# Optimization experiments

Hardware: AMD Instinct MI355X
Metric: run time of the kernel (lower is better)

The kernel has to match this reference:

```python
import jax, jax.numpy as jnp
import numpy as np
from jax.ops import segment_sum

HID = 64
B = 512  # number of graphs


def gcn(x, W, b, src, dst, n):
    # PyG GCNConv: h = xW; add self-loops; symmetric norm D^-1/2 A_hat D^-1/2; + bias
    h = x @ W
    deg = 1.0 + segment_sum(jnp.ones_like(src, dtype=h.dtype), dst, num_segments=n)
    dinv = deg ** -0.5
    msg = h[src] * (dinv[src] * dinv[dst])[:, None]          # [E, out]
    out = segment_sum(msg, dst, num_segments=n) + h * (dinv * dinv)[:, None]
    return out + b


def mean_pool(x, batch, nb):
    s = segment_sum(x, batch, num_segments=nb)
    cnt = segment_sum(jnp.ones_like(batch, dtype=x.dtype), batch, num_segments=nb)
    return s / jnp.maximum(cnt, 1.0)[:, None]


def branch(x, ei, batch, params):
    (W1, b1, W2, b2, W3, b3) = params
    n = x.shape[0]
    src, dst = ei[0], ei[1]
    x = jax.nn.relu(gcn(x, W1, b1, src, dst, n))
    x = jax.nn.relu(gcn(x, W2, b2, src, dst, n))
    x = jax.nn.relu(gcn(x, W3, b3, src, dst, n))
    return mean_pool(x, batch, B)


def setup_inputs() -> dict:
    key = jax.random.key(0)
    ks = jax.random.split(key, 24)
    s = 0.05
    d = {
        'p_x': jax.random.normal(ks[0], (200000, 41), jnp.float32),
        'p_edge_index': jax.random.randint(ks[1], (2, 800000), 0, 200000, jnp.int32),
        'p_batch': jnp.sort(jax.random.randint(ks[2], (200000,), 0, B, jnp.int32)),
        'l_x': jax.random.normal(ks[3], (100000, 78), jnp.float32),
        'l_edge_index': jax.random.randint(ks[4], (2, 400000), 0, 100000, jnp.int32),
        'l_batch': jnp.sort(jax.random.randint(ks[5], (100000,), 0, B, jnp.int32)),
    }
    def lin(k, i, o):
        return jax.random.normal(k, (i, o), jnp.float32) * s
    d['p_W1'] = lin(ks[6], 41, HID);      d['p_b1'] = jnp.zeros((HID,))
    d['p_W2'] = lin(ks[7], HID, 2*HID);   d['p_b2'] = jnp.zeros((2*HID,))
    d['p_W3'] = lin(ks[8], 2*HID, 4*HID); d['p_b3'] = jnp.zeros((4*HID,))
    d['l_W1'] = lin(ks[9], 78, HID);      d['l_b1'] = jnp.zeros((HID,))
    d['l_W2'] = lin(ks[10], HID, 2*HID);  d['l_b2'] = jnp.zeros((2*HID,))
    d['l_W3'] = lin(ks[11], 2*HID, 4*HID); d['l_b3'] = jnp.zeros((4*HID,))
    d['fc1_W'] = lin(ks[12], 8*HID, 1024); d['fc1_b'] = jnp.zeros((1024,))
    d['fc2_W'] = lin(ks[13], 1024, 512);   d['fc2_b'] = jnp.zeros((512,))
    d['out_W'] = lin(ks[14], 512, 1);      d['out_b'] = jnp.zeros((1,))
    return d


def reference(p_x, p_edge_index, p_batch, l_x, l_edge_index, l_batch,
              p_W1, p_b1, p_W2, p_b2, p_W3, p_b3,
              l_W1, l_b1, l_W2, l_b2, l_W3, l_b3,
              fc1_W, fc1_b, fc2_W, fc2_b, out_W, out_b):
    p = branch(p_x, p_edge_index, p_batch, (p_W1, p_b1, p_W2, p_b2, p_W3, p_b3))
    l = branch(l_x, l_edge_index, l_batch, (l_W1, l_b1, l_W2, l_b2, l_W3, l_b3))
    x = jnp.concatenate([p, l], axis=1)                      # [B, 512]
    x = jax.nn.relu(x @ fc1_W + fc1_b)
    # dropout is identity in eval mode
    x = jax.nn.relu(x @ fc2_W + fc2_b)
    return x @ out_W + out_b                                  # [B, 1]
```

## Files before the change

### kernel.cpp

```cpp
#include <hip/hip_runtime.h>

typedef __attribute__((ext_vector_type(8))) short short8;
typedef __attribute__((ext_vector_type(16))) float f32x16;


__device__ __forceinline__ unsigned short f2bf_rne(float f) {
  unsigned u = __float_as_uint(f);
  u += 0x7fffu + ((u >> 16) & 1u);
  return (unsigned short)(u >> 16);
}
__device__ __forceinline__ float bf2f(unsigned short h) {
  return __uint_as_float(((unsigned)h) << 16);
}


static __global__ void k_fill(float* __restrict__ p, float v, int n) {
  int i = blockIdx.x * blockDim.x + threadIdx.x;
  if (i < n) p[i] = v;
}

static __global__ void k_deg(float* __restrict__ deg, const int* __restrict__ dst, int E) {
  int e = blockIdx.x * blockDim.x + threadIdx.x;
  if (e < E) atomicAdd(&deg[dst[e]], 1.0f);
}

static __global__ void k_count_sorted(float* __restrict__ cnt, const int* __restrict__ batch,
                                      int n, int nb) {
  int b = blockIdx.x * blockDim.x + threadIdx.x;
  if (b >= nb) return;
  int lo = 0, hi = n;
  while (lo < hi) { int mid = (lo + hi) >> 1; if (batch[mid] < b) lo = mid + 1; else hi = mid; }
  int start = lo;
  lo = 0; hi = n;
  while (lo < hi) { int mid = (lo + hi) >> 1; if (batch[mid] < b + 1) lo = mid + 1; else hi = mid; }
  cnt[b] = (float)(lo - start);
}


static __global__ void k_scan1(const float* __restrict__ degf, int* __restrict__ ex,
                               int* __restrict__ bsum, int n) {
  __shared__ int sm[256];
  int i = blockIdx.x * 256 + threadIdx.x;
  int v = (i < n) ? ((int)degf[i] - 1) : 0;
  sm[threadIdx.x] = v;
  __syncthreads();
  for (int off = 1; off < 256; off <<= 1) {
    int t = (threadIdx.x >= (unsigned)off) ? sm[threadIdx.x - off] : 0;
    __syncthreads();
    sm[threadIdx.x] += t;
    __syncthreads();
  }
  if (i < n) ex[i] = sm[threadIdx.x] - v;
  if (threadIdx.x == 255) bsum[blockIdx.x] = sm[255];
}

static __global__ void k_scan2(int* __restrict__ bsum, int nb) {
  __shared__ int sm[1024];
  __shared__ int carry;
  if (threadIdx.x == 0) carry = 0;
  __syncthreads();
  for (int base = 0; base < nb; base += 1024) {
    int i = base + threadIdx.x;
    int v = (i < nb) ? bsum[i] : 0;
    sm[threadIdx.x] = v;
    __syncthreads();
    for (int off = 1; off < 1024; off <<= 1) {
      int t = (threadIdx.x >= (unsigned)off) ? sm[threadIdx.x - off] : 0;
      __syncthreads();
      sm[threadIdx.x] += t;
      __syncthreads();
    }
    if (i < nb) bsum[i] = sm[threadIdx.x] + carry;
    __syncthreads();
    if (threadIdx.x == 0) carry += sm[1023];
    __syncthreads();
  }
}

static __global__ void k_scan3(int* __restrict__ rowptr, int* __restrict__ cursor_ex,
                               const int* __restrict__ bsum, float* __restrict__ dinv,
                               int n, int E) {
  int i = blockIdx.x * 256 + threadIdx.x;
  if (i > n) return;
  if (i == n) { rowptr[n] = E; return; }
  int add = blockIdx.x ? bsum[blockIdx.x - 1] : 0;
  int r = cursor_ex[i] + add;
  rowptr[i] = r;
  cursor_ex[i] = r;
  dinv[i] = 1.0f / sqrtf(dinv[i]);
}

static __global__ void k_fill_csr(const int* __restrict__ src, const int* __restrict__ dst,
                                  int* __restrict__ cursor, int* __restrict__ esrc, int E) {
  int e = blockIdx.x * 256 + threadIdx.x;
  if (e >= E) return;
  int pos = atomicAdd(&cursor[dst[e]], 1);
  esrc[pos] = src[e];
}

static __global__ void __launch_bounds__(256)
k_agg(float* __restrict__ AG, const float* __restrict__ X,
      const int* __restrict__ rowptr, const int* __restrict__ esrc,
      const float* __restrict__ dinv, int n, int K) {
  int wid = (blockIdx.x * blockDim.x + threadIdx.x) >> 6;
  int lane = threadIdx.x & 63;
  if (wid >= n) return;
  int rs = rowptr[wid], re = rowptr[wid + 1];
  float dv = dinv[wid];
  const float* xr = X + (size_t)wid * K;
  float a0 = (lane < K) ? xr[lane] * dv * dv : 0.0f;
  float a1 = (64 + lane < K) ? xr[64 + lane] * dv * dv : 0.0f;
  for (int e = rs; e < re; ++e) {
    int s = esrc[e];
    float w = dinv[s] * dv;
    const float* xs = X + (size_t)s * K;
    if (lane < K) a0 = fmaf(xs[lane], w, a0);
    if (64 + lane < K) a1 = fmaf(xs[64 + lane], w, a1);
  }
  float* ar = AG + (size_t)wid * K;
  if (lane < K) ar[lane] = a0;
  if (64 + lane < K) ar[64 + lane] = a1;
}

template<int LG>
static __global__ void __launch_bounds__(256)
k_agg_split(unsigned short* __restrict__ AGh, unsigned short* __restrict__ AGl,
            const float* __restrict__ X,
            const int* __restrict__ rowptr, const int* __restrict__ esrc,
            const float* __restrict__ dinv, int n) {
  const int K = (1 << LG) * 4;
  int gid = (blockIdx.x * blockDim.x + threadIdx.x) >> LG;
  int gl = threadIdx.x & ((1 << LG) - 1);
  if (gid >= n) return;
  int rs = rowptr[gid], re = rowptr[gid + 1];
  float dv = dinv[gid];
  float4 a = *(const float4*)(X + (size_t)gid * K + gl * 4);
  float dv2 = dv * dv;
  a.x *= dv2; a.y *= dv2; a.z *= dv2; a.w *= dv2;
  for (int e = rs; e < re; ++e) {
    int s = esrc[e];
    float w = dinv[s] * dv;
    float4 xs = *(const float4*)(X + (size_t)s * K + gl * 4);
    a.x = fmaf(xs.x, w, a.x);
    a.y = fmaf(xs.y, w, a.y);
    a.z = fmaf(xs.z, w, a.z);
    a.w = fmaf(xs.w, w, a.w);
  }
  size_t base = (size_t)gid * K + gl * 4;
  unsigned short h0 = f2bf_rne(a.x), h1 = f2bf_rne(a.y), h2 = f2bf_rne(a.z), h3 = f2bf_rne(a.w);
  ushort4 hv = {h0, h1, h2, h3};
  ushort4 lv = {f2bf_rne(a.x - bf2f(h0)), f2bf_rne(a.y - bf2f(h1)),
                f2bf_rne(a.z - bf2f(h2)), f2bf_rne(a.w - bf2f(h3))};
  *(ushort4*)&AGh[base] = hv;
  *(ushort4*)&AGl[base] = lv;
}

static __global__ void k_wsplit(const float* __restrict__ W,
                                unsigned short* __restrict__ Wth, unsigned short* __restrict__ Wtl,
                                int Kin, int Kout) {
  int idx = blockIdx.x * blockDim.x + threadIdx.x;
  if (idx >= Kin * Kout) return;
  int k = idx / Kout, c = idx - k * Kout;
  float v = W[idx];
  unsigned short h = f2bf_rne(v);
  Wth[(size_t)c * Kin + k] = h;
  Wtl[(size_t)c * Kin + k] = f2bf_rne(v - bf2f(h));
}

template<bool POOL>
static __global__ void __launch_bounds__(256)
k_gemm_mfma(const unsigned short* __restrict__ Ah, const unsigned short* __restrict__ Al,
            const unsigned short* __restrict__ Bth, const unsigned short* __restrict__ Btl,
            const float* __restrict__ bias, float* __restrict__ Y,
            int n, int K, int Kout,
            const int* __restrict__ batch, int ystride, int colbase) {
  __shared__ __align__(16) unsigned short sAh[128 * 32];
  __shared__ __align__(16) unsigned short sAl[128 * 32];
  __shared__ __align__(16) unsigned short sBh[128 * 32];
  __shared__ __align__(16) unsigned short sBl[128 * 32];

  const int tid = threadIdx.x;
  const int lane = tid & 63;
  const int wid = tid >> 6;
  const int wr = wid >> 1, wc = wid & 1;
  const int g = lane >> 5;
  const int r0 = blockIdx.x * 128;
  const int c0 = blockIdx.y * 128;

  f32x16 acc[2][2] = {};

  const int srow = tid & 127;
  const int q0 = tid >> 7;

  const int nch = K / 32;
  for (int ch = 0; ch < nch; ++ch) {
    const int k0 = ch * 32;
    if (ch) __syncthreads();
    {
      bool rok = (r0 + srow) < n;
      size_t abase = (size_t)(r0 + srow) * K + k0;
      size_t bbase = (size_t)(c0 + srow) * K + k0;
      int swz = ((srow >> 1) & 3) << 3;
#pragma unroll
      for (int qq = 0; qq < 2; ++qq) {
        int q = q0 + 2 * qq;
        int sidx = srow * 32 + ((q * 8) ^ swz);
        short8 vh = {}, vl = {};
        if (rok) {
          vh = *(const short8*)&Ah[abase + q * 8];
          vl = *(const short8*)&Al[abase + q * 8];
        }
        *(short8*)&sAh[sidx] = vh;
        *(short8*)&sAl[sidx] = vl;
        *(short8*)&sBh[sidx] = *(const short8*)&Bth[bbase + q * 8];
        *(short8*)&sBl[sidx] = *(const short8*)&Btl[bbase + q * 8];
      }
    }
    __syncthreads();
#pragma unroll
    for (int kk = 0; kk < 2; ++kk) {
      short8 ah[2], al[2], bh[2], bl[2];
#pragma unroll
      for (int f = 0; f < 2; ++f) {
        int ra = wr * 64 + f * 32 + (lane & 31);
        int ka = (kk * 16 + g * 8) ^ (((ra >> 1) & 3) << 3);
        ah[f] = *(const short8*)&sAh[ra * 32 + ka];
        al[f] = *(const short8*)&sAl[ra * 32 + ka];
        int rb = wc * 64 + f * 32 + (lane & 31);
        int kb = (kk * 16 + g * 8) ^ (((rb >> 1) & 3) << 3);
        bh[f] = *(const short8*)&sBh[rb * 32 + kb];
        bl[f] = *(const short8*)&sBl[rb * 32 + kb];
      }
#pragma unroll
      for (int fa = 0; fa < 2; ++fa)
#pragma unroll
        for (int fb = 0; fb < 2; ++fb) {
          acc[fa][fb] = __builtin_amdgcn_mfma_f32_32x32x16_bf16(ah[fa], bh[fb], acc[fa][fb], 0, 0, 0);
          acc[fa][fb] = __builtin_amdgcn_mfma_f32_32x32x16_bf16(ah[fa], bl[fb], acc[fa][fb], 0, 0, 0);
          acc[fa][fb] = __builtin_amdgcn_mfma_f32_32x32x16_bf16(al[fa], bh[fb], acc[fa][fb], 0, 0, 0);
        }
    }
  }

  if (!POOL) {
#pragma unroll
    for (int fa = 0; fa < 2; ++fa)
#pragma unroll
      for (int fb = 0; fb < 2; ++fb) {
        int col = c0 + wc * 64 + fb * 32 + (lane & 31);
        float bcol = bias[col];
#pragma unroll
        for (int r = 0; r < 16; ++r) {
          int grow = r0 + wr * 64 + fa * 32 + (r & 3) + 8 * (r >> 2) + 4 * g;
          if (grow < n) {
            float v = fmaxf(acc[fa][fb][r] + bcol, 0.0f);
            Y[(size_t)grow * ystride + col] = v;
          }
        }
      }
  } else {
#pragma unroll
    for (int fa = 0; fa < 2; ++fa)
#pragma unroll
      for (int fb = 0; fb < 2; ++fb) {
        int col = colbase + c0 + wc * 64 + fb * 32 + (lane & 31);
        float bcol = bias[c0 + wc * 64 + fb * 32 + (lane & 31)];
        float s = 0.0f;
        int cur = -1;
#pragma unroll
        for (int r = 0; r < 16; ++r) {
          int grow = r0 + wr * 64 + fa * 32 + (r & 3) + 8 * (r >> 2) + 4 * g;
          if (grow < n) {
            int b = batch[grow];
            if (b != cur) {
              if (cur >= 0 && s != 0.0f)
                atomicAdd(&Y[(size_t)cur * ystride + col], s);
              cur = b;
              s = 0.0f;
            }
            s += fmaxf(acc[fa][fb][r] + bcol, 0.0f);
          }
        }
        if (cur >= 0 && s != 0.0f)
          atomicAdd(&Y[(size_t)cur * ystride + col], s);
      }
  }
}

template<bool RELU>
static __global__ void __launch_bounds__(256)
k_gemm_t(const float* __restrict__ A, const float* __restrict__ W,
         const float* __restrict__ bias, float* __restrict__ Y,
         int n, int Kin, int Kout, int ystride) {
  __shared__ float As[32][68];
  __shared__ float Ws[32][68];

  const int tid = threadIdx.x;
  const int tx = tid & 15, ty = tid >> 4;
  const int r0 = blockIdx.x * 64;
  const int c0 = blockIdx.y * 64;

  float acc[4][4] = {};

  const int ar = tid & 63;
  const int akg = (tid >> 6) * 8;
  const int wkk = tid & 31;
  const int wcg = (tid >> 5) * 8;

  const int nch = (Kin + 31) / 32;
  for (int ch = 0; ch < nch; ++ch) {
    const int k0 = ch * 32;
    {
      int grow = r0 + ar;
      bool rok = grow < n;
      const float* arow = A + (size_t)grow * Kin;
#pragma unroll
      for (int i = 0; i < 8; ++i) {
        int k = k0 + akg + i;
        As[akg + i][ar] = (rok && k < Kin) ? arow[k] : 0.0f;
      }
    }
    {
      int gk = k0 + wkk;
      float4 v0 = make_float4(0.f, 0.f, 0.f, 0.f), v1 = v0;
      if (gk < Kin) {
        const float* wp = W + (size_t)gk * Kout + c0 + wcg;
        v0 = *(const float4*)wp;
        v1 = *(const float4*)(wp + 4);
      }
      *(float4*)&Ws[wkk][wcg] = v0;
      *(float4*)&Ws[wkk][wcg + 4] = v1;
    }
    __syncthreads();
#pragma unroll
    for (int k = 0; k < 32; ++k) {
      float4 a4 = *(const float4*)&As[k][ty * 4];
      float4 w4 = *(const float4*)&Ws[k][tx * 4];
      float av[4] = {a4.x, a4.y, a4.z, a4.w};
      float wv[4] = {w4.x, w4.y, w4.z, w4.w};
#pragma unroll
      for (int i = 0; i < 4; ++i)
#pragma unroll
        for (int j = 0; j < 4; ++j)
          acc[i][j] = fmaf(av[i], wv[j], acc[i][j]);
    }
    __syncthreads();
  }

  float4 bv = *(const float4*)&bias[c0 + tx * 4];
  float bb[4] = {bv.x, bv.y, bv.z, bv.w};
#pragma unroll
  for (int i = 0; i < 4; ++i) {
    int row = r0 + ty * 4 + i;
    if (row < n) {
      float o[4];
#pragma unroll
      for (int j = 0; j < 4; ++j) {
        o[j] = acc[i][j] + bb[j];
        if (RELU) o[j] = fmaxf(o[j], 0.0f);
      }
      *(float4*)&Y[(size_t)row * ystride + c0 + tx * 4] = make_float4(o[0], o[1], o[2], o[3]);
    }
  }
}

static __global__ void k_pool_div(float* __restrict__ pooled, const float* __restrict__ cnt,
                                  int colbase) {
  int i = blockIdx.x * blockDim.x + threadIdx.x;
  if (i >= 512 * 256) return;
  int b = i >> 8;
  int c = i & 255;
  pooled[b * 512 + colbase + c] /= fmaxf(cnt[b], 1.0f);
}

static __global__ void k_out(float* __restrict__ out, const float* __restrict__ X,
                             const float* __restrict__ w, const float* __restrict__ b) {
  int row = blockIdx.x;
  int lane = threadIdx.x;
  float acc = 0.f;
  for (int k = lane; k < 512; k += 64)
    acc = fmaf(X[row * 512 + k], w[k], acc);
#pragma unroll
  for (int off = 32; off; off >>= 1) acc += __shfl_down(acc, off);
  if (lane == 0) out[row] = acc + b[0];
}


extern "C" void kernel_launch(void* const* d_in, const int* in_sizes, int n_in,
                              void* d_out, int out_size, void* d_ws, size_t ws_size,
                              hipStream_t stream) {
  const float* p_x  = (const float*)d_in[0];
  const int*   p_ei = (const int*)d_in[1];
  const int*   p_bt = (const int*)d_in[2];
  const float* l_x  = (const float*)d_in[3];
  const int*   l_ei = (const int*)d_in[4];
  const int*   l_bt = (const int*)d_in[5];
  const float* pW1 = (const float*)d_in[6],  *pb1 = (const float*)d_in[7];
  const float* pW2 = (const float*)d_in[8],  *pb2 = (const float*)d_in[9];
  const float* pW3 = (const float*)d_in[10], *pb3 = (const float*)d_in[11];
  const float* lW1 = (const float*)d_in[12], *lb1 = (const float*)d_in[13];
  const float* lW2 = (const float*)d_in[14], *lb2 = (const float*)d_in[15];
  const float* lW3 = (const float*)d_in[16], *lb3 = (const float*)d_in[17];
  const float* fc1W = (const float*)d_in[18], *fc1b = (const float*)d_in[19];
  const float* fc2W = (const float*)d_in[20], *fc2b = (const float*)d_in[21];
  const float* oW  = (const float*)d_in[22], *ob  = (const float*)d_in[23];

  const int n_p = in_sizes[2], n_l = in_sizes[5];
  const int E_p = in_sizes[1] / 2, E_l = in_sizes[4] / 2;
  const int IN_P = in_sizes[0] / n_p, IN_L = in_sizes[3] / n_l;

  char* wsc = (char*)d_ws;
  size_t off = 0;
  auto alloc = [&](size_t bytes) -> void* {
    void* p = wsc + off;
    off = (off + bytes + 255) & ~(size_t)255;
    return p;
  };
  float* dinv_p = (float*)alloc((size_t)n_p * 4);
  float* dinv_l = (float*)alloc((size_t)n_l * 4);
  float* cnt_p  = (float*)alloc(512 * 4);
  float* cnt_l  = (float*)alloc(512 * 4);
  float* pooled = (float*)alloc(512 * 512 * 4);
  float* F      = (float*)alloc((size_t)n_p * 128 * 4);
  unsigned short* AGh = (unsigned short*)alloc((size_t)n_p * 128 * 2);
  unsigned short* AGl = (unsigned short*)alloc((size_t)n_p * 128 * 2);
  float* AGf    = (float*)AGh;
  unsigned short* W2th = (unsigned short*)alloc(64 * 128 * 2);
  unsigned short* W2tl = (unsigned short*)alloc(64 * 128 * 2);
  unsigned short* W3th = (unsigned short*)alloc(128 * 256 * 2);
  unsigned short* W3tl = (unsigned short*)alloc(128 * 256 * 2);
  int* bsum     = (int*)alloc(1024 * 4);
  int* cur_p    = (int*)alloc((size_t)n_p * 4);
  int* row_p    = (int*)alloc(((size_t)n_p + 1) * 4);
  int* esrc_p   = (int*)alloc((size_t)E_p * 4);
  int* cur_l    = (int*)alloc((size_t)n_l * 4);
  int* row_l    = (int*)alloc(((size_t)n_l + 1) * 4);
  int* esrc_l   = (int*)alloc((size_t)E_l * 4);
  float* fc1o   = F;
  float* fc2o   = F + 512 * 1024;
  (void)ws_size; (void)n_in; (void)out_size;

  hipMemsetAsync(pooled, 0, 512 * 512 * 4, stream);

  auto gemm64 = [&](const float* A, const float* W, const float* b, float* Y,
                    int n, int Kin, int Kout, int ystride) {
    dim3 grd((n + 63) / 64, Kout / 64);
    k_gemm_t<true><<<grd, 256, 0, stream>>>(A, W, b, Y, n, Kin, Kout, ystride);
  };

  auto branch = [&](const float* x0, const int* ei, const int* batch, int n, int E, int IN,
                    const float* W1, const float* b1, const float* W2, const float* b2,
                    const float* W3, const float* b3, float* dinv, float* cnt,
                    int* cursor, int* rowptr, int* esrc, int colbase) {
    const int* src = ei;
    const int* dst = ei + E;
    const int nb = (n + 255) / 256;
    k_fill<<<nb, 256, 0, stream>>>(dinv, 1.0f, n);
    k_deg<<<(E + 255) / 256, 256, 0, stream>>>(dinv, dst, E);
    k_count_sorted<<<2, 256, 0, stream>>>(cnt, batch, n, 512);
    k_scan1<<<nb, 256, 0, stream>>>(dinv, cursor, bsum, n);
    k_scan2<<<1, 1024, 0, stream>>>(bsum, nb);
    k_scan3<<<(n + 256) / 256 + 1, 256, 0, stream>>>(rowptr, cursor, bsum, dinv, n, E);
    k_fill_csr<<<(E + 255) / 256, 256, 0, stream>>>(src, dst, cursor, esrc, E);
    k_wsplit<<<(64 * 128 + 255) / 256, 256, 0, stream>>>(W2, W2th, W2tl, 64, 128);
    k_wsplit<<<(128 * 256 + 255) / 256, 256, 0, stream>>>(W3, W3th, W3tl, 128, 256);
    k_agg<<<(n * 64 + 255) / 256, 256, 0, stream>>>(AGf, x0, rowptr, esrc, dinv, n, IN);
    gemm64(AGf, W1, b1, F, n, IN, 64, 64);
    k_agg_split<4><<<(n * 16 + 255) / 256, 256, 0, stream>>>(AGh, AGl, F, rowptr, esrc, dinv, n);
    {
      dim3 grd((n + 127) / 128, 1);
      k_gemm_mfma<false><<<grd, 256, 0, stream>>>(AGh, AGl, W2th, W2tl, b2, F,
                                                  n, 64, 128, nullptr, 128, 0);
    }
    k_agg_split<5><<<(n * 32 + 255) / 256, 256, 0, stream>>>(AGh, AGl, F, rowptr, esrc, dinv, n);
    {
      dim3 grd((n + 127) / 128, 2);
      k_gemm_mfma<true><<<grd, 256, 0, stream>>>(AGh, AGl, W3th, W3tl, b3, pooled,
                                                 n, 128, 256, batch, 512, colbase);
    }
  };

  branch(p_x, p_ei, p_bt, n_p, E_p, IN_P, pW1, pb1, pW2, pb2, pW3, pb3,
         dinv_p, cnt_p, cur_p, row_p, esrc_p, 0);
  branch(l_x, l_ei, l_bt, n_l, E_l, IN_L, lW1, lb1, lW2, lb2, lW3, lb3,
         dinv_l, cnt_l, cur_l, row_l, esrc_l, 256);

  k_pool_div<<<(512 * 256 + 255) / 256, 256, 0, stream>>>(pooled, cnt_p, 0);
  k_pool_div<<<(512 * 256 + 255) / 256, 256, 0, stream>>>(pooled, cnt_l, 256);

  gemm64(pooled, fc1W, fc1b, fc1o, 512, 512, 1024, 1024);
  gemm64(fc1o, fc2W, fc2b, fc2o, 512, 1024, 512, 512);
  k_out<<<512, 64, 0, stream>>>((float*)d_out, fc2o, oW, ob);
}
```

Measured before the change: 1.281 ms.

## Pre-tile bf16 operands into MFMA fragment layout and drop LDS staging

The aggregation and weight-split kernels now write their hi/lo bf16 outputs in a blocked layout of 32 rows by 8-element k-chunks. This matches the per-lane fragments of the 32x32x16 MFMA. The GEMM kernel is templated on K and loads fragments straight from global memory, removing the shared-memory copies, swizzling and barriers. The cost is less regular store coalescing in the aggregation kernels. The A buffers are padded to a multiple of 128 rows, and the padded rows stay uninitialized but are masked at output.

```diff
diff --git a/kernel.cpp b/kernel.cpp
--- a/kernel.cpp
+++ b/kernel.cpp
@@ -129,6 +129,7 @@
             const int* __restrict__ rowptr, const int* __restrict__ esrc,
             const float* __restrict__ dinv, int n) {
   const int K = (1 << LG) * 4;
+  const int NCH = K / 8;
   int gid = (blockIdx.x * blockDim.x + threadIdx.x) >> LG;
   int gl = threadIdx.x & ((1 << LG) - 1);
   if (gid >= n) return;
@@ -146,7 +147,10 @@
     a.z = fmaf(xs.z, w, a.z);
     a.w = fmaf(xs.w, w, a.w);
   }
-  size_t base = (size_t)gid * K + gl * 4;
+  int rb = gid >> 5, r = gid & 31;
+  int c = gl >> 1;
+  int half = (gl & 1) * 4;
+  size_t base = (((size_t)rb * NCH + c) * 32 + r) * 8 + half;
   unsigned short h0 = f2bf_rne(a.x), h1 = f2bf_rne(a.y), h2 = f2bf_rne(a.z), h3 = f2bf_rne(a.w);
   ushort4 hv = {h0, h1, h2, h3};
   ushort4 lv = {f2bf_rne(a.x - bf2f(h0)), f2bf_rne(a.y - bf2f(h1)),
@@ -163,83 +167,55 @@
   int k = idx / Kout, c = idx - k * Kout;
   float v = W[idx];
   unsigned short h = f2bf_rne(v);
-  Wth[(size_t)c * Kin + k] = h;
-  Wtl[(size_t)c * Kin + k] = f2bf_rne(v - bf2f(h));
-}
-
-template<bool POOL>
+  int cb = c >> 5, c31 = c & 31, ch = k >> 3, k7 = k & 7;
+  size_t base = (((size_t)cb * (Kin / 8) + ch) * 32 + c31) * 8 + k7;
+  Wth[base] = h;
+  Wtl[base] = f2bf_rne(v - bf2f(h));
+}
+
+template<int K, bool POOL>
 static __global__ void __launch_bounds__(256)
 k_gemm_mfma(const unsigned short* __restrict__ Ah, const unsigned short* __restrict__ Al,
             const unsigned short* __restrict__ Bth, const unsigned short* __restrict__ Btl,
             const float* __restrict__ bias, float* __restrict__ Y,
-            int n, int K, int Kout,
+            int n, int Kout,
             const int* __restrict__ batch, int ystride, int colbase) {
-  __shared__ __align__(16) unsigned short sAh[128 * 32];
-  __shared__ __align__(16) unsigned short sAl[128 * 32];
-  __shared__ __align__(16) unsigned short sBh[128 * 32];
-  __shared__ __align__(16) unsigned short sBl[128 * 32];
-
+  const int NCH = K / 8;
+  const int NKK = K / 16;
   const int tid = threadIdx.x;
   const int lane = tid & 63;
   const int wid = tid >> 6;
   const int wr = wid >> 1, wc = wid & 1;
   const int g = lane >> 5;
+  const int l31 = lane & 31;
   const int r0 = blockIdx.x * 128;
   const int c0 = blockIdx.y * 128;
+  const int rb0 = (r0 >> 5) + wr * 2;
+  const int cb0 = (c0 >> 5) + wc * 2;
 
   f32x16 acc[2][2] = {};
 
-  const int srow = tid & 127;
-  const int q0 = tid >> 7;
-
-  const int nch = K / 32;
-  for (int ch = 0; ch < nch; ++ch) {
-    const int k0 = ch * 32;
-    if (ch) __syncthreads();
-    {
-      bool rok = (r0 + srow) < n;
-      size_t abase = (size_t)(r0 + srow) * K + k0;
-      size_t bbase = (size_t)(c0 + srow) * K + k0;
-      int swz = ((srow >> 1) & 3) << 3;
-#pragma unroll
-      for (int qq = 0; qq < 2; ++qq) {
-        int q = q0 + 2 * qq;
-        int sidx = srow * 32 + ((q * 8) ^ swz);
-        short8 vh = {}, vl = {};
-        if (rok) {
-          vh = *(const short8*)&Ah[abase + q * 8];
-          vl = *(const short8*)&Al[abase + q * 8];
-        }
-        *(short8*)&sAh[sidx] = vh;
-        *(short8*)&sAl[sidx] = vl;
-        *(short8*)&sBh[sidx] = *(const short8*)&Bth[bbase + q * 8];
-        *(short8*)&sBl[sidx] = *(const short8*)&Btl[bbase + q * 8];
-      }
-    }
-    __syncthreads();
-#pragma unroll
-    for (int kk = 0; kk < 2; ++kk) {
-      short8 ah[2], al[2], bh[2], bl[2];
-#pragma unroll
-      for (int f = 0; f < 2; ++f) {
-        int ra = wr * 64 + f * 32 + (lane & 31);
-        int ka = (kk * 16 + g * 8) ^ (((ra >> 1) & 3) << 3);
-        ah[f] = *(const short8*)&sAh[ra * 32 + ka];
-        al[f] = *(const short8*)&sAl[ra * 32 + ka];
-        int rb = wc * 64 + f * 32 + (lane & 31);
-        int kb = (kk * 16 + g * 8) ^ (((rb >> 1) & 3) << 3);
-        bh[f] = *(const short8*)&sBh[rb * 32 + kb];
-        bl[f] = *(const short8*)&sBl[rb * 32 + kb];
-      }
-#pragma unroll
-      for (int fa = 0; fa < 2; ++fa)
-#pragma unroll
-        for (int fb = 0; fb < 2; ++fb) {
-          acc[fa][fb] = __builtin_amdgcn_mfma_f32_32x32x16_bf16(ah[fa], bh[fb], acc[fa][fb], 0, 0, 0);
-          acc[fa][fb] = __builtin_amdgcn_mfma_f32_32x32x16_bf16(ah[fa], bl[fb], acc[fa][fb], 0, 0, 0);
-          acc[fa][fb] = __builtin_amdgcn_mfma_f32_32x32x16_bf16(al[fa], bh[fb], acc[fa][fb], 0, 0, 0);
-        }
-    }
+#pragma unroll
+  for (int kk = 0; kk < NKK; ++kk) {
+    const int ch = 2 * kk + g;
+    short8 ah[2], al[2], bh[2], bl[2];
+#pragma unroll
+    for (int f = 0; f < 2; ++f) {
+      size_t aoff = (((size_t)(rb0 + f) * NCH + ch) * 32 + l31) * 8;
+      ah[f] = *(const short8*)&Ah[aoff];
+      al[f] = *(const short8*)&Al[aoff];
+      size_t boff = (((size_t)(cb0 + f) * NCH + ch) * 32 + l31) * 8;
+      bh[f] = *(const short8*)&Bth[boff];
+      bl[f] = *(const short8*)&Btl[boff];
+    }
+#pragma unroll
+    for (int fa = 0; fa < 2; ++fa)
+#pragma unroll
+      for (int fb = 0; fb < 2; ++fb) {
+        acc[fa][fb] = __builtin_amdgcn_mfma_f32_32x32x16_bf16(ah[fa], bh[fb], acc[fa][fb], 0, 0, 0);
+        acc[fa][fb] = __builtin_amdgcn_mfma_f32_32x32x16_bf16(ah[fa], bl[fb], acc[fa][fb], 0, 0, 0);
+        acc[fa][fb] = __builtin_amdgcn_mfma_f32_32x32x16_bf16(al[fa], bh[fb], acc[fa][fb], 0, 0, 0);
+      }
   }
 
   if (!POOL) {
@@ -247,7 +223,7 @@
     for (int fa = 0; fa < 2; ++fa)
 #pragma unroll
       for (int fb = 0; fb < 2; ++fb) {
-        int col = c0 + wc * 64 + fb * 32 + (lane & 31);
+        int col = c0 + wc * 64 + fb * 32 + l31;
         float bcol = bias[col];
 #pragma unroll
         for (int r = 0; r < 16; ++r) {
@@ -263,8 +239,8 @@
     for (int fa = 0; fa < 2; ++fa)
 #pragma unroll
       for (int fb = 0; fb < 2; ++fb) {
-        int col = colbase + c0 + wc * 64 + fb * 32 + (lane & 31);
-        float bcol = bias[c0 + wc * 64 + fb * 32 + (lane & 31)];
+        int col = colbase + c0 + wc * 64 + fb * 32 + l31;
+        float bcol = bias[c0 + wc * 64 + fb * 32 + l31];
         float s = 0.0f;
         int cur = -1;
 #pragma unroll
@@ -408,6 +384,7 @@
   const int n_p = in_sizes[2], n_l = in_sizes[5];
   const int E_p = in_sizes[1] / 2, E_l = in_sizes[4] / 2;
   const int IN_P = in_sizes[0] / n_p, IN_L = in_sizes[3] / n_l;
+  const int nr_p = (n_p + 127) & ~127;
 
   char* wsc = (char*)d_ws;
   size_t off = 0;
@@ -422,8 +399,8 @@
   float* cnt_l  = (float*)alloc(512 * 4);
   float* pooled = (float*)alloc(512 * 512 * 4);
   float* F      = (float*)alloc((size_t)n_p * 128 * 4);
-  unsigned short* AGh = (unsigned short*)alloc((size_t)n_p * 128 * 2);
-  unsigned short* AGl = (unsigned short*)alloc((size_t)n_p * 128 * 2);
+  unsigned short* AGh = (unsigned short*)alloc((size_t)nr_p * 128 * 2);
+  unsigned short* AGl = (unsigned short*)alloc((size_t)nr_p * 128 * 2);
   float* AGf    = (float*)AGh;
   unsigned short* W2th = (unsigned short*)alloc(64 * 128 * 2);
   unsigned short* W2tl = (unsigned short*)alloc(64 * 128 * 2);
@@ -469,14 +446,14 @@
     k_agg_split<4><<<(n * 16 + 255) / 256, 256, 0, stream>>>(AGh, AGl, F, rowptr, esrc, dinv, n);
     {
       dim3 grd((n + 127) / 128, 1);
-      k_gemm_mfma<false><<<grd, 256, 0, stream>>>(AGh, AGl, W2th, W2tl, b2, F,
-                                                  n, 64, 128, nullptr, 128, 0);
+      k_gemm_mfma<64, false><<<grd, 256, 0, stream>>>(AGh, AGl, W2th, W2tl, b2, F,
+                                                      n, 128, nullptr, 128, 0);
     }
     k_agg_split<5><<<(n * 32 + 255) / 256, 256, 0, stream>>>(AGh, AGl, F, rowptr, esrc, dinv, n);
     {
       dim3 grd((n + 127) / 128, 2);
-      k_gemm_mfma<true><<<grd, 256, 0, stream>>>(AGh, AGl, W3th, W3tl, b3, pooled,
-                                                 n, 128, 256, batch, 512, colbase);
+      k_gemm_mfma<128, true><<<grd, 256, 0, stream>>>(AGh, AGl, W3th, W3tl, b3, pooled,
+                                                      n, 256, batch, 512, colbase);
     }
   };
 
```

Measured after the change: 1.200 ms. 1.07x faster.
